# Optimization experiments

Hardware: AMD Instinct MI355X
Metric: run time of the kernel (lower is better)

Reference implementation:

```python
import jax, jax.numpy as jnp
import numpy as np

H, D = 8, 64
LN_EPS = 1e-5

def elu_p1(x):
    return jax.nn.elu(x) + 1.0

def sum_norm(x):
    return x / jnp.sum(x, axis=-1, keepdims=True)

def setup_inputs() -> dict:
    key = jax.random.key(0)
    k1, k2, k3 = jax.random.split(key, 3)
    slen, bsz, in_dim = 1024, 32, 512
    x = jax.random.normal(k1, (slen, bsz, in_dim), dtype=jnp.float32)
    ln_gamma = jnp.ones((in_dim,), dtype=jnp.float32)
    ln_beta = jnp.zeros((in_dim,), dtype=jnp.float32)
    # Linear weights stored as [in, out] (transposed vs torch) and fan-in scaled
    w_slow = jax.random.normal(k2, (in_dim, H * (3 * D + 1)), dtype=jnp.float32) / np.sqrt(in_dim)
    w_out = jax.random.normal(k3, (H * D, in_dim), dtype=jnp.float32) / np.sqrt(H * D)
    return {"x": x, "ln_gamma": ln_gamma, "ln_beta": ln_beta, "w_slow": w_slow, "w_out": w_out}

def reference(x, ln_gamma, ln_beta, w_slow, w_out):
    slen, bsz, in_dim = x.shape
    # LayerNorm
    mu = jnp.mean(x, axis=-1, keepdims=True)
    var = jnp.mean((x - mu) ** 2, axis=-1, keepdims=True)
    h = (x - mu) * jax.lax.rsqrt(var + LN_EPS) * ln_gamma + ln_beta
    # slow net projection -> q, k, v, beta per head
    qkvb = (h @ w_slow).reshape(slen, bsz, H, 3 * D + 1)
    q, k, v, beta = jnp.split(qkvb, [D, 2 * D, 3 * D], axis=-1)
    beta = jax.nn.sigmoid(beta)            # [slen, bsz, H, 1]
    q = sum_norm(elu_p1(q))                # [slen, bsz, H, D]
    k = sum_norm(elu_p1(k))
    # delta-rule fast-weight recurrence over time
    W0 = jnp.zeros((bsz, H, D, D), dtype=x.dtype)
    def step(W, inp):
        q_t, k_t, v_t, b_t = inp           # [bsz,H,D], [bsz,H,D], [bsz,H,D], [bsz,H,1]
        v_old = jnp.einsum('bhij,bhj->bhi', W, k_t)
        upd = b_t * (v_t - v_old)          # [bsz,H,D]
        W = W + upd[..., :, None] * k_t[..., None, :]
        o_t = jnp.einsum('bhij,bhj->bhi', W, q_t)
        return W, o_t
    _, outs = jax.lax.scan(step, W0, (q, k, v, beta))  # outs [slen, bsz, H, D]
    out = outs.reshape(slen, bsz, H * D) @ w_out       # [slen, bsz, in_dim]
    return x + out
```

## Files before the change

kernel.cpp:

```cpp
#include <hip/hip_runtime.h>
#include <cstdint>

using short8  = __attribute__((ext_vector_type(8))) short;
using ushort8 = __attribute__((ext_vector_type(8))) unsigned short;
using short4v = __attribute__((ext_vector_type(4))) short;
using f32x4   = __attribute__((ext_vector_type(4))) float;

#define H_    8
#define SLEN  1024
#define BSZ   32
#define INDIM 512
#define NQKV  1544
#define NPAD2 1792
#define MROWS 32768
#define PB    72

#define GLOAD16(gp, lp) __builtin_amdgcn_global_load_lds( \
    (const __attribute__((address_space(1))) void*)(gp),  \
    (__attribute__((address_space(3))) void*)(lp), 16, 0, 0)

#define VMCNT8() do { asm volatile("s_waitcnt vmcnt(8)" ::: "memory"); \
                      __builtin_amdgcn_sched_barrier(0); } while (0)
#define VMCNT0() do { asm volatile("s_waitcnt vmcnt(0)" ::: "memory"); \
                      __builtin_amdgcn_sched_barrier(0); } while (0)
#define SBAR()   do { __builtin_amdgcn_sched_barrier(0); \
                      __builtin_amdgcn_s_barrier(); \
                      __builtin_amdgcn_sched_barrier(0); } while (0)

static __device__ __forceinline__ float bf2f(unsigned short s) {
    return __uint_as_float(((unsigned int)s) << 16);
}
#if defined(__BF16_MANT_DIG__)
static __device__ __forceinline__ unsigned short f2bf(float f) {
    union { __bf16 b; unsigned short u; } cv;
    cv.b = (__bf16)f;
    return cv.u;
}
#else
static __device__ __forceinline__ unsigned short f2bf(float f) {
    unsigned int u = __float_as_uint(f);
    u += 0x7FFFu + ((u >> 16) & 1u);
    return (unsigned short)(u >> 16);
}
#endif

__global__ __launch_bounds__(256) void ln_kernel(const float* __restrict__ x,
                                                 const float* __restrict__ gamma,
                                                 const float* __restrict__ betap,
                                                 unsigned short* __restrict__ h) {
    int row = blockIdx.x * 4 + (threadIdx.x >> 6);
    int l   = threadIdx.x & 63;
    const f32x4* xr = (const f32x4*)(x + (size_t)row * INDIM);
    f32x4 a = xr[l * 2], b = xr[l * 2 + 1];
    float s = 0.f, sq = 0.f;
    #pragma unroll
    for (int j = 0; j < 4; ++j) { s += a[j]; sq += a[j] * a[j]; }
    #pragma unroll
    for (int j = 0; j < 4; ++j) { s += b[j]; sq += b[j] * b[j]; }
    #pragma unroll
    for (int off = 32; off; off >>= 1) { s += __shfl_xor(s, off); sq += __shfl_xor(sq, off); }
    float mean = s * (1.f / 512.f);
    float var  = sq * (1.f / 512.f) - mean * mean;
    float rstd = rsqrtf(var + 1e-5f);
    const f32x4* g4 = (const f32x4*)gamma;
    const f32x4* b4 = (const f32x4*)betap;
    f32x4 g0 = g4[l * 2], g1 = g4[l * 2 + 1], e0 = b4[l * 2], e1 = b4[l * 2 + 1];
    short8 o;
    #pragma unroll
    for (int j = 0; j < 4; ++j) o[j]     = (short)f2bf((a[j] - mean) * rstd * g0[j] + e0[j]);
    #pragma unroll
    for (int j = 0; j < 4; ++j) o[4 + j] = (short)f2bf((b[j] - mean) * rstd * g1[j] + e1[j]);
    ((short8*)(h + (size_t)row * INDIM))[l] = o;
}

__global__ __launch_bounds__(256) void cvt_wslow2(const float* __restrict__ w,
                                                  unsigned short* __restrict__ wT) {
    __shared__ float T[64][65];
    const int tid = threadIdx.x;
    const int k0 = blockIdx.x * 64;
    const int ng = blockIdx.y;
    if (ng < 24) {
        const int cbase = (ng & 7) * 193 + (ng >> 3) * 64;
        const int nn = tid & 63, kk = tid >> 6;
        #pragma unroll
        for (int i = 0; i < 16; ++i)
            T[kk + 4 * i][nn] = w[(size_t)(k0 + kk + 4 * i) * NQKV + cbase + nn];
        __syncthreads();
        const int kseg = (tid & 7) * 8;
        #pragma unroll
        for (int i = 0; i < 2; ++i) {
            int nn2 = i * 32 + (tid >> 3);
            ushort8 o;
            #pragma unroll
            for (int j = 0; j < 8; ++j) o[j] = f2bf(T[kseg + j][nn2]);
            *(ushort8*)&wT[(size_t)(ng * 64 + nn2) * 512 + k0 + kseg] = o;
        }
    } else {
        for (int i = 0; i < 64; ++i) {
            int gid = i * 256 + tid;
            int nn = gid >> 6, kk = gid & 63;
            int n = 1536 + nn;
            unsigned short v = 0;
            if (n < 1544) v = f2bf(w[(size_t)(k0 + kk) * NQKV + (n - 1536) * 193 + 192]);
            wT[(size_t)n * 512 + k0 + kk] = v;
        }
    }
}
__global__ __launch_bounds__(256) void cvt_wout(const float* __restrict__ w,
                                                unsigned short* __restrict__ wT) {
    __shared__ float T[64][65];
    const int tid = threadIdx.x;
    const int k0 = blockIdx.x * 64;
    const int n0 = blockIdx.y * 64;
    const int nn = tid & 63, kk = tid >> 6;
    #pragma unroll
    for (int i = 0; i < 16; ++i)
        T[kk + 4 * i][nn] = w[(size_t)(k0 + kk + 4 * i) * 512 + n0 + nn];
    __syncthreads();
    const int kseg = (tid & 7) * 8;
    #pragma unroll
    for (int i = 0; i < 2; ++i) {
        int nn2 = i * 32 + (tid >> 3);
        ushort8 o;
        #pragma unroll
        for (int j = 0; j < 8; ++j) o[j] = f2bf(T[kseg + j][nn2]);
        *(ushort8*)&wT[(size_t)(n0 + nn2) * 512 + k0 + kseg] = o;
    }
}

__global__ __launch_bounds__(512, 2) void gemm_qkv(const unsigned short* __restrict__ A,
                                                   const unsigned short* __restrict__ BT,
                                                   unsigned short* __restrict__ qn,
                                                   unsigned short* __restrict__ kn,
                                                   unsigned short* __restrict__ vn,
                                                   float* __restrict__ bet) {
    __shared__ unsigned short SMEM[65536];
    const int tid = threadIdx.x;
    const int id = blockIdx.y * 7 + blockIdx.x;
    const int newid = (id & 7) * 112 + (id >> 3);
    const int bx = newid % 7;
    const int n0 = bx * 256;
    const int m0 = (newid / 7) * 256;
    const int w = tid >> 6, l = tid & 63;
    const int wm = w >> 2, wn = w & 3;
    const int lr = l & 15, lk8 = (l >> 4) * 8;
    f32x4 acc[8][4] = {};

    auto STAGE = [&](int buf, int kt) {
        #pragma unroll
        for (int c2 = 0; c2 < 4; ++c2) {
            int idx = c2 * 512 + tid;
            int row = idx >> 3, kc2 = (idx & 7) * 8;
            int lb = (c2 * 512 + (tid & 448)) * 8;
            GLOAD16(A  + (size_t)(m0 + row) * INDIM + kt + kc2, &SMEM[buf * 16384 + lb]);
            GLOAD16(BT + (size_t)(n0 + row) * INDIM + kt + kc2, &SMEM[32768 + buf * 16384 + lb]);
        }
    };
    auto COMPUTE = [&](int buf) {
        const unsigned short* As = &SMEM[buf * 16384];
        const unsigned short* Bs = &SMEM[32768 + buf * 16384];
        short8 bf2[4][2];
        #pragma unroll
        for (int ni = 0; ni < 4; ++ni)
            #pragma unroll
            for (int kk = 0; kk < 2; ++kk)
                bf2[ni][kk] = *(const short8*)&Bs[(wn * 64 + ni * 16 + lr) * 64 + kk * 32 + lk8];
        #pragma unroll
        for (int p = 0; p < 4; ++p) {
            short8 af[2][2];
            #pragma unroll
            for (int d = 0; d < 2; ++d)
                #pragma unroll
                for (int kk = 0; kk < 2; ++kk)
                    af[d][kk] = *(const short8*)&As[(wm * 128 + (2 * p + d) * 16 + lr) * 64 + kk * 32 + lk8];
            #pragma unroll
            for (int d = 0; d < 2; ++d)
                #pragma unroll
                for (int ni = 0; ni < 4; ++ni)
                    #pragma unroll
                    for (int kk = 0; kk < 2; ++kk)
                        acc[2 * p + d][ni] =
                            __builtin_amdgcn_mfma_f32_16x16x32_bf16(af[d][kk], bf2[ni][kk], acc[2 * p + d][ni], 0, 0, 0);
        }
    };

    STAGE(0, 0);
    STAGE(1, 64);
    #pragma unroll
    for (int tp = 0; tp < 4; ++tp) {
        VMCNT8();
        SBAR();
        COMPUTE(0);
        SBAR();
        if (tp < 3) {
            STAGE(0, (2 * tp + 2) * 64);
            VMCNT8();
        } else {
            VMCNT0();
        }
        SBAR();
        COMPUTE(1);
        SBAR();
        if (tp < 3) STAGE(1, (2 * tp + 3) * 64);
    }

    const int g = l >> 4, cc = l & 15;
    const int colbase = n0 + wn * 64;
    if (bx < 6) {
        const int reg = colbase >> 9;
        #pragma unroll
        for (int mi = 0; mi < 8; ++mi) {
            #pragma unroll
            for (int j = 0; j < 4; ++j) {
                float e0 = acc[mi][0][j], e1 = acc[mi][1][j], e2 = acc[mi][2][j], e3 = acc[mi][3][j];
                if (reg < 2) {
                    e0 = e0 > 0.f ? e0 + 1.f : __expf(e0);
                    e1 = e1 > 0.f ? e1 + 1.f : __expf(e1);
                    e2 = e2 > 0.f ? e2 + 1.f : __expf(e2);
                    e3 = e3 > 0.f ? e3 + 1.f : __expf(e3);
                    float ssum = (e0 + e1) + (e2 + e3);
                    ssum += __shfl_xor(ssum, 1);
                    ssum += __shfl_xor(ssum, 2);
                    ssum += __shfl_xor(ssum, 4);
                    ssum += __shfl_xor(ssum, 8);
                    float inv = 1.f / ssum;
                    e0 *= inv; e1 *= inv; e2 *= inv; e3 *= inv;
                }
                int lrow = wm * 128 + mi * 16 + g * 4 + j;
                int key = ((lrow >> 2) & 3) << 4;
                int cb = wn * 64;
                SMEM[lrow * 256 + ((cb +  0 + cc) ^ key)] = f2bf(e0);
                SMEM[lrow * 256 + ((cb + 16 + cc) ^ key)] = f2bf(e1);
                SMEM[lrow * 256 + ((cb + 32 + cc) ^ key)] = f2bf(e2);
                SMEM[lrow * 256 + ((cb + 48 + cc) ^ key)] = f2bf(e3);
            }
        }
        SBAR();
        unsigned short* dst = (reg == 0) ? qn : (reg == 1) ? kn : vn;
        #pragma unroll
        for (int it = 0; it < 16; ++it) {
            int idx = it * 512 + tid;
            int lrow = idx >> 5, seg = idx & 31;
            int key = ((lrow >> 2) & 3) << 4;
            ushort8 v = *(const ushort8*)&SMEM[lrow * 256 + ((seg * 8) ^ key)];
            int grow = m0 + lrow;
            int s = grow >> 5, b = grow & 31;
            int gcol = n0 + seg * 8;
            int hd = (gcol >> 6) & 7, d0 = gcol & 63;
            *(ushort8*)(dst + ((size_t)(b * H_ + hd) * SLEN + s) * 64 + d0) = v;
        }
    } else {
        if (wn == 0 && cc < 8) {
            #pragma unroll
            for (int mi = 0; mi < 8; ++mi)
                #pragma unroll
                for (int j = 0; j < 4; ++j) {
                    int row = m0 + wm * 128 + mi * 16 + g * 4 + j;
                    int s = row >> 5, b = row & 31;
                    float v = acc[mi][0][j];
                    bet[(size_t)(b * H_ + cc) * SLEN + s] = 1.f / (1.f + __expf(-v));
                }
        }
    }
}

__global__ __launch_bounds__(512, 2) void gemm_out(const unsigned short* __restrict__ A,
                                                   const unsigned short* __restrict__ BT,
                                                   const float* __restrict__ X,
                                                   float* __restrict__ outf) {
    __shared__ unsigned short As[2][256 * 64];
    __shared__ unsigned short Bs[2][256 * 64];
    const int tid = threadIdx.x;
    const int id = blockIdx.y * 2 + blockIdx.x;
    const int newid = (id & 7) * 32 + (id >> 3);
    const int n0 = (newid & 1) * 256;
    const int m0 = (newid >> 1) * 256;
    const int w = tid >> 6, l = tid & 63;
    const int wm = w >> 2, wn = w & 3;
    const int lr = l & 15, lk8 = (l >> 4) * 8;
    f32x4 acc[8][4] = {};

    auto STAGE = [&](int buf, int kt) {
        #pragma unroll
        for (int c2 = 0; c2 < 4; ++c2) {
            int idx = c2 * 512 + tid;
            int row = idx >> 3, kc2 = (idx & 7) * 8;
            int lb = (c2 * 512 + (tid & 448)) * 8;
            GLOAD16(A  + (size_t)(m0 + row) * INDIM + kt + kc2, &As[buf][lb]);
            GLOAD16(BT + (size_t)(n0 + row) * INDIM + kt + kc2, &Bs[buf][lb]);
        }
    };
    auto COMPUTE = [&](int buf) {
        short8 bf2[4][2];
        #pragma unroll
        for (int ni = 0; ni < 4; ++ni)
            #pragma unroll
            for (int kk = 0; kk < 2; ++kk)
                bf2[ni][kk] = *(const short8*)&Bs[buf][(wn * 64 + ni * 16 + lr) * 64 + kk * 32 + lk8];
        #pragma unroll
        for (int p = 0; p < 4; ++p) {
            short8 af[2][2];
            #pragma unroll
            for (int d = 0; d < 2; ++d)
                #pragma unroll
                for (int kk = 0; kk < 2; ++kk)
                    af[d][kk] = *(const short8*)&As[buf][(wm * 128 + (2 * p + d) * 16 + lr) * 64 + kk * 32 + lk8];
            #pragma unroll
            for (int d = 0; d < 2; ++d)
                #pragma unroll
                for (int ni = 0; ni < 4; ++ni)
                    #pragma unroll
                    for (int kk = 0; kk < 2; ++kk)
                        acc[2 * p + d][ni] =
                            __builtin_amdgcn_mfma_f32_16x16x32_bf16(af[d][kk], bf2[ni][kk], acc[2 * p + d][ni], 0, 0, 0);
        }
    };

    STAGE(0, 0);
    STAGE(1, 64);
    #pragma unroll
    for (int tp = 0; tp < 4; ++tp) {
        VMCNT8();
        SBAR();
        COMPUTE(0);
        SBAR();
        if (tp < 3) {
            STAGE(0, (2 * tp + 2) * 64);
            VMCNT8();
        } else {
            VMCNT0();
        }
        SBAR();
        COMPUTE(1);
        SBAR();
        if (tp < 3) STAGE(1, (2 * tp + 3) * 64);
    }

    const int g = l >> 4, cc = l & 15;
    #pragma unroll
    for (int mi = 0; mi < 8; ++mi)
        #pragma unroll
        for (int ni = 0; ni < 4; ++ni)
            #pragma unroll
            for (int j = 0; j < 4; ++j) {
                int row = m0 + wm * 128 + mi * 16 + g * 4 + j;
                int col = n0 + wn * 64 + ni * 16 + cc;
                size_t o = (size_t)row * 512 + col;
                outf[o] = X[o] + acc[mi][ni][j];
            }
}

__global__ __launch_bounds__(512, 4) void fwtiles(const unsigned short* __restrict__ qn,
                                                  const unsigned short* __restrict__ kn,
                                                  const unsigned short* __restrict__ vn,
                                                  const float* __restrict__ beta,
                                                  unsigned short* __restrict__ tiles,
                                                  unsigned short* __restrict__ outs) {
    __shared__ unsigned short Ax[64 * PB], Atr[64 * PB], Pw[64 * PB], Pwtr[64 * PB];
    __shared__ unsigned short Z0[128 * PB], Z1[128 * PB];
    __shared__ float bv[64];
    const int bx = blockIdx.x;
    const int bh = bx >> 4, c = bx & 15;
    const int b = bh >> 3, h = bh & 7;
    const int c0 = c * 64;
    const int tid = threadIdx.x;
    const int w = tid >> 6, l = tid & 63;
    const int mw = w & 3, nh = w >> 2;
    const int lr = l & 15, lk = (l >> 4) << 3, rb = (l >> 4) << 2;
    const unsigned short* kc = kn + ((size_t)bh * SLEN + c0) * 64;
    const unsigned short* qc = qn + ((size_t)bh * SLEN + c0) * 64;
    const unsigned short* vc = vn + ((size_t)bh * SLEN + c0) * 64;
    const float* bb = beta + (size_t)bh * SLEN + c0;

    {
        #pragma unroll
        for (int i = 0; i < 2; ++i) {
            int idx = i * 512 + tid;
            int row = idx >> 3, seg = idx & 7;
            const unsigned short* src = (row < 64) ? (vc + (size_t)row * 64 + seg * 8)
                                                   : (kc + (size_t)(row - 64) * 64 + seg * 8);
            *(ushort8*)&Z1[row * PB + seg * 8] = *(const ushort8*)src;
        }
        if (tid < 64) bv[tid] = bb[tid];
        ushort8 z8 = {};
        for (int i = tid; i < 576; i += 512) { ((ushort8*)Ax)[i] = z8; ((ushort8*)Atr)[i] = z8; }
    }
    __syncthreads();

    auto ldb = [&](const unsigned short* M, int m, int kk) -> short8 {
        return *(const short8*)&M[(m * 16 + lr) * PB + kk * 32 + lk];
    };

    {
        const int zoff2 = (w >> 2) * 64;
        const int tbase = (w & 3) * 16;
        const float sgn = (w >= 4) ? -1.f : 1.f;
        ushort8 b0v, b1v;
        #pragma unroll
        for (int i = 0; i < 16; ++i) {
            int r = w * 16 + i;
            float val = sgn * bv[tbase + i] * bf2f(Z1[r * PB + l]);
            unsigned short uv = f2bf(val);
            if (i < 8) b0v[i] = uv; else b1v[i - 8] = uv;
        }
        *(ushort8*)&Z0[(zoff2 + l) * PB + tbase]     = b0v;
        *(ushort8*)&Z0[(zoff2 + l) * PB + tbase + 8] = b1v;
    }
    {
        const int pm[10] = {0, 1, 1, 2, 2, 2, 3, 3, 3, 3};
        const int pn[10] = {0, 0, 1, 0, 1, 2, 0, 1, 2, 3};
        for (int pi = w; pi < 10; pi += 8) {
            int m = pm[pi], n = pn[pi];
            short8 ka0 = *(const short8*)&Z1[(64 + 16 * m + lr) * PB + lk];
            short8 ka1 = *(const short8*)&Z1[(64 + 16 * m + lr) * PB + 32 + lk];
            short8 kb0 = *(const short8*)&Z1[(64 + 16 * n + lr) * PB + lk];
            short8 kb1 = *(const short8*)&Z1[(64 + 16 * n + lr) * PB + 32 + lk];
            f32x4 a = {};
            a = __builtin_amdgcn_mfma_f32_16x16x32_bf16(ka0, kb0, a, 0, 0, 0);
            a = __builtin_amdgcn_mfma_f32_16x16x32_bf16(ka1, kb1, a, 0, 0, 0);
            f32x4 btm = *(const f32x4*)&bv[16 * m + rb];
            short4v pk;
            #pragma unroll
            for (int j = 0; j < 4; ++j) {
                int tt = 16 * m + rb + j, s = 16 * n + lr;
                unsigned short v = (s < tt) ? f2bf(-btm[j] * a[j]) : (unsigned short)0;
                Ax[tt * PB + s] = v;
                pk[j] = (short)v;
            }
            *(short4v*)&Atr[(16 * n + lr) * PB + 16 * m + rb] = pk;
        }
    }
    __syncthreads();

    auto zprod = [&](const unsigned short* Xb, int p, const unsigned short* Zs, unsigned short* Zd) {
        const bool msk0 = (16 * mw + 15 >= p), msk1 = (16 * mw + 15 - 32 >= p);
        short8 xf0, xf1;
        if (msk0) xf0 = ldb(Xb, mw, 0);
        if (msk1) xf1 = ldb(Xb, mw, 1);
        #pragma unroll
        for (int ni = 0; ni < 4; ++ni) {
            int n = nh * 4 + ni;
            short4v zi = *(const short4v*)&Zs[(16 * n + lr) * PB + 16 * mw + rb];
            f32x4 a;
            #pragma unroll
            for (int j = 0; j < 4; ++j) a[j] = bf2f((unsigned short)zi[j]);
            if (msk0) a = __builtin_amdgcn_mfma_f32_16x16x32_bf16(xf0, ldb(Zs, n, 0), a, 0, 0, 0);
            if (msk1) a = __builtin_amdgcn_mfma_f32_16x16x32_bf16(xf1, ldb(Zs, n, 1), a, 0, 0, 0);
            short4v zo;
            #pragma unroll
            for (int j = 0; j < 4; ++j) zo[j] = (short)f2bf(a[j]);
            *(short4v*)&Zd[(16 * n + lr) * PB + 16 * mw + rb] = zo;
        }
    };
    auto powp = [&](const unsigned short* Ps, const unsigned short* Pstr, int p,
                    unsigned short* Pd, unsigned short* Pdtr, bool wrTr) {
        const bool x0 = (16 * mw + 15 >= p), x1 = (16 * mw + 15 - 32 >= p);
        short8 xf0, xf1;
        if (x0) xf0 = ldb(Ps, mw, 0);
        if (x1) xf1 = ldb(Ps, mw, 1);
        #pragma unroll
        for (int ni = 0; ni < 2; ++ni) {
            int n = nh * 2 + ni;
            const bool y0 = (31 - 16 * n >= p), y1 = (63 - 16 * n >= p);
            f32x4 a = {};
            if (x0 && y0) a = __builtin_amdgcn_mfma_f32_16x16x32_bf16(xf0, ldb(Pstr, n, 0), a, 0, 0, 0);
            if (x1 && y1) a = __builtin_amdgcn_mfma_f32_16x16x32_bf16(xf1, ldb(Pstr, n, 1), a, 0, 0, 0);
            short4v pk;
            #pragma unroll
            for (int j = 0; j < 4; ++j) {
                unsigned short v = f2bf(a[j]);
                Pd[(16 * mw + rb + j) * PB + 16 * n + lr] = v;
                pk[j] = (short)v;
            }
            if (wrTr) *(short4v*)&Pdtr[(16 * n + lr) * PB + 16 * mw + rb] = pk;
        }
    };

    zprod(Ax, 1, Z0, Z1);  powp(Ax, Atr, 1, Pw, Pwtr, true);   __syncthreads();
    zprod(Pw, 2, Z1, Z0);  powp(Pw, Pwtr, 2, Ax, Atr, true);   __syncthreads();
    zprod(Ax, 4, Z0, Z1);  powp(Ax, Atr, 4, Pw, Pwtr, true);   __syncthreads();
    zprod(Pw, 8, Z1, Z0);  powp(Pw, Pwtr, 8, Ax, Atr, true);   __syncthreads();
    zprod(Ax, 16, Z0, Z1); powp(Ax, Atr, 16, Pw, Pwtr, false); __syncthreads();
    zprod(Pw, 32, Z1, Z0);
    __syncthreads();

    {
        #pragma unroll
        for (int i = 0; i < 2; ++i) {
            int idx = i * 512 + tid;
            int row = idx >> 3, seg = idx & 7;
            const unsigned short* src = (row < 64) ? (qc + (size_t)row * 64 + seg * 8)
                                                   : (kc + (size_t)(row - 64) * 64 + seg * 8);
            *(ushort8*)&Z1[row * PB + seg * 8] = *(const ushort8*)src;
        }
    }
    __syncthreads();

    {
        short8 qa0 = *(const short8*)&Z1[(16 * mw + lr) * PB + lk];
        short8 qa1 = *(const short8*)&Z1[(16 * mw + lr) * PB + 32 + lk];
        #pragma unroll
        for (int ni = 0; ni < 2; ++ni) {
            int n = nh * 2 + ni;
            short8 kb0 = *(const short8*)&Z1[(64 + 16 * n + lr) * PB + lk];
            short8 kb1 = *(const short8*)&Z1[(64 + 16 * n + lr) * PB + 32 + lk];
            f32x4 a = {};
            a = __builtin_amdgcn_mfma_f32_16x16x32_bf16(qa0, kb0, a, 0, 0, 0);
            a = __builtin_amdgcn_mfma_f32_16x16x32_bf16(qa1, kb1, a, 0, 0, 0);
            #pragma unroll
            for (int j = 0; j < 4; ++j) {
                int tt = 16 * mw + rb + j, s = 16 * n + lr;
                Ax[tt * PB + s] = (s <= tt) ? f2bf(a[j]) : (unsigned short)0;
            }
        }
        ushort8 kv;
        #pragma unroll
        for (int j = 0; j < 8; ++j)
            kv[j] = Z1[(64 + w * 8 + j) * PB + l];
        *(ushort8*)&Pwtr[l * PB + w * 8] = kv;
    }
    __syncthreads();

    {
        unsigned short* tb = tiles + ((size_t)bh * 16 + c) * 12288;
        short8 pA0 = ldb(Ax, mw, 0), pA1 = ldb(Ax, mw, 1);
        short8 zA0 = ldb(Z0, mw, 0), zA1 = ldb(Z0, mw, 1);
        short8 kt0 = ldb(Pwtr, mw, 0), kt1 = ldb(Pwtr, mw, 1);
        #pragma unroll
        for (int ni = 0; ni < 2; ++ni) {
            int n = nh * 2 + ni;
            f32x4 aN = {};
            aN = __builtin_amdgcn_mfma_f32_16x16x32_bf16(zA0, ldb(Pwtr, n, 0), aN, 0, 0, 0);
            aN = __builtin_amdgcn_mfma_f32_16x16x32_bf16(zA1, ldb(Pwtr, n, 1), aN, 0, 0, 0);
            f32x4 aM = {};
            aM = __builtin_amdgcn_mfma_f32_16x16x32_bf16(kt0, ldb(Z0, 4 + n, 0), aM, 0, 0, 0);
            aM = __builtin_amdgcn_mfma_f32_16x16x32_bf16(kt1, ldb(Z0, 4 + n, 1), aM, 0, 0, 0);
            f32x4 aG;
            #pragma unroll
            for (int j = 0; j < 4; ++j) aG[j] = bf2f(Z1[(16 * mw + rb + j) * PB + 16 * n + lr]);
            aG = __builtin_amdgcn_mfma_f32_16x16x32_bf16(pA0, ldb(Z0, 4 + n, 0), aG, 0, 0, 0);
            aG = __builtin_amdgcn_mfma_f32_16x16x32_bf16(pA1, ldb(Z0, 4 + n, 1), aG, 0, 0, 0);
            f32x4 aP = {};
            aP = __builtin_amdgcn_mfma_f32_16x16x32_bf16(pA0, ldb(Z0, n, 0), aP, 0, 0, 0);
            aP = __builtin_amdgcn_mfma_f32_16x16x32_bf16(pA1, ldb(Z0, n, 1), aP, 0, 0, 0);
            #pragma unroll
            for (int j = 0; j < 4; ++j) {
                int r = 16 * mw + rb + j, cl = 16 * n + lr;
                tb[r * 64 + cl]        = f2bf(aM[j]);
                tb[4096 + r * 64 + cl] = f2bf(aG[j]);
                tb[8192 + r * 64 + cl] = f2bf(aN[j]);
                outs[((size_t)(c0 + r) * BSZ + b) * 512 + h * 64 + cl] = f2bf(aP[j]);
            }
        }
    }
}

__global__ __launch_bounds__(256) void fwscan_w(const unsigned short* __restrict__ tiles,
                                                unsigned short* __restrict__ wchk) {
    __shared__ float Wf[64 * 68];
    const int bh = blockIdx.x;
    const int tid = threadIdx.x;
    const int w = tid >> 6, l = tid & 63;
    const int lr = l & 15, lk = (l >> 4) << 3, rb = (l >> 4) << 2;
    const int cr = l >> 3, cc8 = (l & 7) * 8;
    #pragma unroll
    for (int j = 0; j < 16; ++j) Wf[(16 * w + j) * 68 + l] = 0.f;

    const unsigned short* tb0 = tiles + (size_t)bh * 16 * 12288;
    unsigned short* wc0 = wchk + (size_t)bh * 16 * 4096;

    auto loadc = [&](short8 (&MT)[4][2], unsigned short (&NV)[4][4], int c) {
        const unsigned short* tb = tb0 + (size_t)c * 12288;
        #pragma unroll
        for (int n = 0; n < 4; ++n) {
            MT[n][0] = *(const short8*)(tb + (size_t)(16 * n + lr) * 64 + lk);
            MT[n][1] = *(const short8*)(tb + (size_t)(16 * n + lr) * 64 + 32 + lk);
            #pragma unroll
            for (int j = 0; j < 4; ++j)
                NV[n][j] = tb[8192 + (size_t)(16 * w + rb + j) * 64 + 16 * n + lr];
        }
    };
    auto stepc = [&](short8 (&MT)[4][2], unsigned short (&NV)[4][4], int c) {
        #pragma unroll
        for (int half = 0; half < 2; ++half) {
            int row = 16 * w + half * 8 + cr;
            const float* p = &Wf[row * 68 + cc8];
            f32x4 x0 = *(const f32x4*)p, x1 = *(const f32x4*)(p + 4);
            ushort8 o;
            #pragma unroll
            for (int j = 0; j < 4; ++j) { o[j] = f2bf(x0[j]); o[4 + j] = f2bf(x1[j]); }
            *(ushort8*)(wc0 + (size_t)c * 4096 + row * 64 + cc8) = o;
        }
        short8 wf0, wf1;
        {
            const float* p0 = &Wf[(16 * w + lr) * 68 + lk];
            f32x4 a0 = *(const f32x4*)p0, b0 = *(const f32x4*)(p0 + 4);
            f32x4 a1 = *(const f32x4*)(p0 + 32), b1 = *(const f32x4*)(p0 + 36);
            #pragma unroll
            for (int j = 0; j < 4; ++j) {
                wf0[j] = (short)f2bf(a0[j]); wf0[4 + j] = (short)f2bf(b0[j]);
                wf1[j] = (short)f2bf(a1[j]); wf1[4 + j] = (short)f2bf(b1[j]);
            }
        }
        #pragma unroll
        for (int n = 0; n < 4; ++n) {
            f32x4 a;
            #pragma unroll
            for (int j = 0; j < 4; ++j)
                a[j] = Wf[(16 * w + rb + j) * 68 + 16 * n + lr] + bf2f(NV[n][j]);
            a = __builtin_amdgcn_mfma_f32_16x16x32_bf16(wf0, MT[n][0], a, 0, 0, 0);
            a = __builtin_amdgcn_mfma_f32_16x16x32_bf16(wf1, MT[n][1], a, 0, 0, 0);
            #pragma unroll
            for (int j = 0; j < 4; ++j) Wf[(16 * w + rb + j) * 68 + 16 * n + lr] = a[j];
        }
    };

    short8 mtA[4][2], mtB[4][2];
    unsigned short nvA[4][4], nvB[4][4];
    loadc(mtA, nvA, 0);
    #pragma unroll 1
    for (int cc = 0; cc < 8; ++cc) {
        int c = 2 * cc;
        if (c + 1 < 16) loadc(mtB, nvB, c + 1);
        stepc(mtA, nvA, c);
        if (c + 2 < 16) loadc(mtA, nvA, c + 2);
        stepc(mtB, nvB, c + 1);
    }
}

__global__ __launch_bounds__(256) void fw_o(const unsigned short* __restrict__ tiles,
                                            const unsigned short* __restrict__ wchk,
                                            unsigned short* __restrict__ outs) {
    __shared__ unsigned short Ot[64 * 72];
    const int c = blockIdx.x + 1;
    const int bh = blockIdx.y;
    const int b = bh >> 3, h = bh & 7;
    const int c0 = c * 64;
    const int tid = threadIdx.x;
    const int w = tid >> 6, l = tid & 63;
    const int lr = l & 15, lk = (l >> 4) << 3, rb = (l >> 4) << 2;
    const unsigned short* G  = tiles + ((size_t)bh * 16 + c) * 12288 + 4096;
    const unsigned short* W0 = wchk + ((size_t)bh * 16 + c) * 4096;

    #pragma unroll
    for (int i = 0; i < 2; ++i) {
        int idx = i * 256 + tid;
        int t = idx >> 3, d0 = (idx & 7) * 8;
        *(ushort8*)&Ot[t * 72 + d0] =
            *(const ushort8*)(outs + ((size_t)(c0 + t) * BSZ + b) * 512 + h * 64 + d0);
    }
    __syncthreads();

    short8 g0 = *(const short8*)(G + (size_t)(16 * w + lr) * 64 + lk);
    short8 g1 = *(const short8*)(G + (size_t)(16 * w + lr) * 64 + 32 + lk);
    #pragma unroll
    for (int n = 0; n < 4; ++n) {
        short8 wf0 = *(const short8*)(W0 + (size_t)(16 * n + lr) * 64 + lk);
        short8 wf1 = *(const short8*)(W0 + (size_t)(16 * n + lr) * 64 + 32 + lk);
        f32x4 a;
        #pragma unroll
        for (int j = 0; j < 4; ++j) a[j] = bf2f(Ot[(16 * w + rb + j) * 72 + 16 * n + lr]);
        a = __builtin_amdgcn_mfma_f32_16x16x32_bf16(g0, wf0, a, 0, 0, 0);
        a = __builtin_amdgcn_mfma_f32_16x16x32_bf16(g1, wf1, a, 0, 0, 0);
        #pragma unroll
        for (int j = 0; j < 4; ++j) Ot[(16 * w + rb + j) * 72 + 16 * n + lr] = f2bf(a[j]);
    }
    __syncthreads();

    #pragma unroll
    for (int i = 0; i < 2; ++i) {
        int idx = i * 256 + tid;
        int t = idx >> 3, d0 = (idx & 7) * 8;
        *(ushort8*)(outs + ((size_t)(c0 + t) * BSZ + b) * 512 + h * 64 + d0) =
            *(const ushort8*)&Ot[t * 72 + d0];
    }
}

extern "C" void kernel_launch(void* const* d_in, const int* in_sizes, int n_in,
                              void* d_out, int out_size, void* d_ws, size_t ws_size,
                              hipStream_t stream) {
    const float* x      = (const float*)d_in[0];
    const float* g      = (const float*)d_in[1];
    const float* be     = (const float*)d_in[2];
    const float* w_slow = (const float*)d_in[3];
    const float* w_out  = (const float*)d_in[4];
    float* out = (float*)d_out;
    char* ws = (char*)d_ws;

    unsigned short* h    = (unsigned short*)(ws);
    unsigned short* outs = (unsigned short*)(ws);
    unsigned short* qn   = (unsigned short*)(ws + 33554432);
    unsigned short* wchk = (unsigned short*)(ws + 33554432);
    unsigned short* kn   = (unsigned short*)(ws + 67108864);
    unsigned short* vn   = (unsigned short*)(ws + 100663296);
    float*          bet  = (float*)         (ws + 134217728);
    unsigned short* wsT  = (unsigned short*)(ws + 135266304);
    unsigned short* woT  = (unsigned short*)(ws + 137101312);
    unsigned short* tiles= (unsigned short*)(ws + 137625600);

    if (ws_size < 238288896) return;

    ln_kernel<<<8192, 256, 0, stream>>>(x, g, be, h);
    cvt_wslow2<<<dim3(8, 25), 256, 0, stream>>>(w_slow, wsT);
    cvt_wout<<<dim3(8, 8), 256, 0, stream>>>(w_out, woT);
    gemm_qkv<<<dim3(7, MROWS / 256), 512, 0, stream>>>(h, wsT, qn, kn, vn, bet);
    fwtiles<<<BSZ * H_ * 16, 512, 0, stream>>>(qn, kn, vn, bet, tiles, outs);
    fwscan_w<<<BSZ * H_, 256, 0, stream>>>(tiles, wchk);
    fw_o<<<dim3(15, BSZ * H_), 256, 0, stream>>>(tiles, wchk, outs);
    gemm_out<<<dim3(2, MROWS / 256), 512, 0, stream>>>(outs, woT, x, out);
}
```

Baseline: 339.8 us.

## Halve GEMM K-tile to 32 to cut LDS and raise occupancy

Result: slower. 780.0 us (+129.6%).

```diff
diff --git a/kernel.cpp b/kernel.cpp
--- a/kernel.cpp
+++ b/kernel.cpp
@@ -1,4 +1,5 @@
 #include <hip/hip_runtime.h>
+#include <hip/hip_bf16.h>
 #include <cstdint>
 
 using short8  = __attribute__((ext_vector_type(8))) short;
@@ -19,7 +20,7 @@
     (const __attribute__((address_space(1))) void*)(gp),  \
     (__attribute__((address_space(3))) void*)(lp), 16, 0, 0)
 
-#define VMCNT8() do { asm volatile("s_waitcnt vmcnt(8)" ::: "memory"); \
+#define VMCNT4() do { asm volatile("s_waitcnt vmcnt(4)" ::: "memory"); \
                       __builtin_amdgcn_sched_barrier(0); } while (0)
 #define VMCNT0() do { asm volatile("s_waitcnt vmcnt(0)" ::: "memory"); \
                       __builtin_amdgcn_sched_barrier(0); } while (0)
@@ -30,19 +31,11 @@
 static __device__ __forceinline__ float bf2f(unsigned short s) {
     return __uint_as_float(((unsigned int)s) << 16);
 }
-#if defined(__BF16_MANT_DIG__)
 static __device__ __forceinline__ unsigned short f2bf(float f) {
-    union { __bf16 b; unsigned short u; } cv;
-    cv.b = (__bf16)f;
+    union { __hip_bfloat16 b; unsigned short u; } cv;
+    cv.b = __float2bfloat16(f);
     return cv.u;
 }
-#else
-static __device__ __forceinline__ unsigned short f2bf(float f) {
-    unsigned int u = __float_as_uint(f);
-    u += 0x7FFFu + ((u >> 16) & 1u);
-    return (unsigned short)(u >> 16);
-}
-#endif
 
 __global__ __launch_bounds__(256) void ln_kernel(const float* __restrict__ x,
                                                  const float* __restrict__ gamma,
@@ -128,13 +121,13 @@
     }
 }
 
-__global__ __launch_bounds__(512, 2) void gemm_qkv(const unsigned short* __restrict__ A,
+__global__ __launch_bounds__(512, 4) void gemm_qkv(const unsigned short* __restrict__ A,
                                                    const unsigned short* __restrict__ BT,
                                                    unsigned short* __restrict__ qn,
                                                    unsigned short* __restrict__ kn,
                                                    unsigned short* __restrict__ vn,
                                                    float* __restrict__ bet) {
-    __shared__ unsigned short SMEM[65536];
+    __shared__ unsigned short SMEM[32768];
     const int tid = threadIdx.x;
     const int id = blockIdx.y * 7 + blockIdx.x;
     const int newid = (id & 7) * 112 + (id >> 3);
@@ -148,106 +141,97 @@
 
     auto STAGE = [&](int buf, int kt) {
         #pragma unroll
-        for (int c2 = 0; c2 < 4; ++c2) {
+        for (int c2 = 0; c2 < 2; ++c2) {
             int idx = c2 * 512 + tid;
-            int row = idx >> 3, kc2 = (idx & 7) * 8;
+            int row = idx >> 2, kc2 = (idx & 3) * 8;
             int lb = (c2 * 512 + (tid & 448)) * 8;
-            GLOAD16(A  + (size_t)(m0 + row) * INDIM + kt + kc2, &SMEM[buf * 16384 + lb]);
-            GLOAD16(BT + (size_t)(n0 + row) * INDIM + kt + kc2, &SMEM[32768 + buf * 16384 + lb]);
+            GLOAD16(A  + (size_t)(m0 + row) * INDIM + kt + kc2, &SMEM[buf * 8192 + lb]);
+            GLOAD16(BT + (size_t)(n0 + row) * INDIM + kt + kc2, &SMEM[16384 + buf * 8192 + lb]);
         }
     };
     auto COMPUTE = [&](int buf) {
-        const unsigned short* As = &SMEM[buf * 16384];
-        const unsigned short* Bs = &SMEM[32768 + buf * 16384];
-        short8 bf2[4][2];
+        const unsigned short* As = &SMEM[buf * 8192];
+        const unsigned short* Bs = &SMEM[16384 + buf * 8192];
+        short8 bf2[4];
         #pragma unroll
         for (int ni = 0; ni < 4; ++ni)
-            #pragma unroll
-            for (int kk = 0; kk < 2; ++kk)
-                bf2[ni][kk] = *(const short8*)&Bs[(wn * 64 + ni * 16 + lr) * 64 + kk * 32 + lk8];
+            bf2[ni] = *(const short8*)&Bs[(wn * 64 + ni * 16 + lr) * 32 + lk8];
         #pragma unroll
         for (int p = 0; p < 4; ++p) {
-            short8 af[2][2];
+            short8 af[2];
             #pragma unroll
             for (int d = 0; d < 2; ++d)
-                #pragma unroll
-                for (int kk = 0; kk < 2; ++kk)
-                    af[d][kk] = *(const short8*)&As[(wm * 128 + (2 * p + d) * 16 + lr) * 64 + kk * 32 + lk8];
+                af[d] = *(const short8*)&As[(wm * 128 + (2 * p + d) * 16 + lr) * 32 + lk8];
             #pragma unroll
             for (int d = 0; d < 2; ++d)
                 #pragma unroll
                 for (int ni = 0; ni < 4; ++ni)
-                    #pragma unroll
-                    for (int kk = 0; kk < 2; ++kk)
-                        acc[2 * p + d][ni] =
-                            __builtin_amdgcn_mfma_f32_16x16x32_bf16(af[d][kk], bf2[ni][kk], acc[2 * p + d][ni], 0, 0, 0);
+                    acc[2 * p + d][ni] =
+                        __builtin_amdgcn_mfma_f32_16x16x32_bf16(af[d], bf2[ni], acc[2 * p + d][ni], 0, 0, 0);
         }
     };
 
     STAGE(0, 0);
-    STAGE(1, 64);
-    #pragma unroll
-    for (int tp = 0; tp < 4; ++tp) {
-        VMCNT8();
+    STAGE(1, 32);
+    #pragma unroll
+    for (int t = 0; t < 16; ++t) {
+        if (t == 15) { VMCNT0(); } else { VMCNT4(); }
         SBAR();
-        COMPUTE(0);
+        COMPUTE(t & 1);
         SBAR();
-        if (tp < 3) {
-            STAGE(0, (2 * tp + 2) * 64);
-            VMCNT8();
-        } else {
-            VMCNT0();
-        }
-        SBAR();
-        COMPUTE(1);
-        SBAR();
-        if (tp < 3) STAGE(1, (2 * tp + 3) * 64);
+        if (t + 2 < 16) STAGE(t & 1, (t + 2) * 32);
     }
 
     const int g = l >> 4, cc = l & 15;
     const int colbase = n0 + wn * 64;
     if (bx < 6) {
         const int reg = colbase >> 9;
-        #pragma unroll
-        for (int mi = 0; mi < 8; ++mi) {
-            #pragma unroll
-            for (int j = 0; j < 4; ++j) {
-                float e0 = acc[mi][0][j], e1 = acc[mi][1][j], e2 = acc[mi][2][j], e3 = acc[mi][3][j];
-                if (reg < 2) {
-                    e0 = e0 > 0.f ? e0 + 1.f : __expf(e0);
-                    e1 = e1 > 0.f ? e1 + 1.f : __expf(e1);
-                    e2 = e2 > 0.f ? e2 + 1.f : __expf(e2);
-                    e3 = e3 > 0.f ? e3 + 1.f : __expf(e3);
-                    float ssum = (e0 + e1) + (e2 + e3);
-                    ssum += __shfl_xor(ssum, 1);
-                    ssum += __shfl_xor(ssum, 2);
-                    ssum += __shfl_xor(ssum, 4);
-                    ssum += __shfl_xor(ssum, 8);
-                    float inv = 1.f / ssum;
-                    e0 *= inv; e1 *= inv; e2 *= inv; e3 *= inv;
+        unsigned short* dst = (reg == 0) ? qn : (reg == 1) ? kn : vn;
+        #pragma unroll
+        for (int hp = 0; hp < 2; ++hp) {
+            SBAR();
+            if (wm == hp) {
+                #pragma unroll
+                for (int mi = 0; mi < 8; ++mi) {
+                    #pragma unroll
+                    for (int j = 0; j < 4; ++j) {
+                        float e0 = acc[mi][0][j], e1 = acc[mi][1][j], e2 = acc[mi][2][j], e3 = acc[mi][3][j];
+                        if (reg < 2) {
+                            e0 = e0 > 0.f ? e0 + 1.f : __expf(e0);
+                            e1 = e1 > 0.f ? e1 + 1.f : __expf(e1);
+                            e2 = e2 > 0.f ? e2 + 1.f : __expf(e2);
+                            e3 = e3 > 0.f ? e3 + 1.f : __expf(e3);
+                            float ssum = (e0 + e1) + (e2 + e3);
+                            ssum += __shfl_xor(ssum, 1);
+                            ssum += __shfl_xor(ssum, 2);
+                            ssum += __shfl_xor(ssum, 4);
+                            ssum += __shfl_xor(ssum, 8);
+                            float inv = 1.f / ssum;
+                            e0 *= inv; e1 *= inv; e2 *= inv; e3 *= inv;
+                        }
+                        int lrow = mi * 16 + g * 4 + j;
+                        int key = ((lrow >> 2) & 3) << 4;
+                        int cb = wn * 64;
+                        SMEM[lrow * 256 + ((cb +  0 + cc) ^ key)] = f2bf(e0);
+                        SMEM[lrow * 256 + ((cb + 16 + cc) ^ key)] = f2bf(e1);
+                        SMEM[lrow * 256 + ((cb + 32 + cc) ^ key)] = f2bf(e2);
+                        SMEM[lrow * 256 + ((cb + 48 + cc) ^ key)] = f2bf(e3);
+                    }
                 }
-                int lrow = wm * 128 + mi * 16 + g * 4 + j;
+            }
+            SBAR();
+            #pragma unroll
+            for (int it = 0; it < 8; ++it) {
+                int idx = it * 512 + tid;
+                int lrow = idx >> 5, seg = idx & 31;
                 int key = ((lrow >> 2) & 3) << 4;
-                int cb = wn * 64;
-                SMEM[lrow * 256 + ((cb +  0 + cc) ^ key)] = f2bf(e0);
-                SMEM[lrow * 256 + ((cb + 16 + cc) ^ key)] = f2bf(e1);
-                SMEM[lrow * 256 + ((cb + 32 + cc) ^ key)] = f2bf(e2);
-                SMEM[lrow * 256 + ((cb + 48 + cc) ^ key)] = f2bf(e3);
-            }
-        }
-        SBAR();
-        unsigned short* dst = (reg == 0) ? qn : (reg == 1) ? kn : vn;
-        #pragma unroll
-        for (int it = 0; it < 16; ++it) {
-            int idx = it * 512 + tid;
-            int lrow = idx >> 5, seg = idx & 31;
-            int key = ((lrow >> 2) & 3) << 4;
-            ushort8 v = *(const ushort8*)&SMEM[lrow * 256 + ((seg * 8) ^ key)];
-            int grow = m0 + lrow;
-            int s = grow >> 5, b = grow & 31;
-            int gcol = n0 + seg * 8;
-            int hd = (gcol >> 6) & 7, d0 = gcol & 63;
-            *(ushort8*)(dst + ((size_t)(b * H_ + hd) * SLEN + s) * 64 + d0) = v;
+                ushort8 v = *(const ushort8*)&SMEM[lrow * 256 + ((seg * 8) ^ key)];
+                int grow = m0 + hp * 128 + lrow;
+                int s = grow >> 5, b = grow & 31;
+                int gcol = n0 + seg * 8;
+                int hd = (gcol >> 6) & 7, d0 = gcol & 63;
+                *(ushort8*)(dst + ((size_t)(b * H_ + hd) * SLEN + s) * 64 + d0) = v;
+            }
         }
     } else {
         if (wn == 0 && cc < 8) {
@@ -264,12 +248,12 @@
     }
 }
 
-__global__ __launch_bounds__(512, 2) void gemm_out(const unsigned short* __restrict__ A,
+__global__ __launch_bounds__(512, 4) void gemm_out(const unsigned short* __restrict__ A,
                                                    const unsigned short* __restrict__ BT,
                                                    const float* __restrict__ X,
                                                    float* __restrict__ outf) {
-    __shared__ unsigned short As[2][256 * 64];
-    __shared__ unsigned short Bs[2][256 * 64];
+    __shared__ unsigned short As2[2][8192];
+    __shared__ unsigned short Bs2[2][8192];
     const int tid = threadIdx.x;
     const int id = blockIdx.y * 2 + blockIdx.x;
     const int newid = (id & 7) * 32 + (id >> 3);
@@ -282,58 +266,43 @@
 
     auto STAGE = [&](int buf, int kt) {
         #pragma unroll
-        for (int c2 = 0; c2 < 4; ++c2) {
+        for (int c2 = 0; c2 < 2; ++c2) {
             int idx = c2 * 512 + tid;
-            int row = idx >> 3, kc2 = (idx & 7) * 8;
+            int row = idx >> 2, kc2 = (idx & 3) * 8;
             int lb = (c2 * 512 + (tid & 448)) * 8;
-            GLOAD16(A  + (size_t)(m0 + row) * INDIM + kt + kc2, &As[buf][lb]);
-            GLOAD16(BT + (size_t)(n0 + row) * INDIM + kt + kc2, &Bs[buf][lb]);
+            GLOAD16(A  + (size_t)(m0 + row) * INDIM + kt + kc2, &As2[buf][lb]);
+            GLOAD16(BT + (size_t)(n0 + row) * INDIM + kt + kc2, &Bs2[buf][lb]);
         }
     };
     auto COMPUTE = [&](int buf) {
-        short8 bf2[4][2];
+        short8 bf2[4];
         #pragma unroll
         for (int ni = 0; ni < 4; ++ni)
-            #pragma unroll
-            for (int kk = 0; kk < 2; ++kk)
-                bf2[ni][kk] = *(const short8*)&Bs[buf][(wn * 64 + ni * 16 + lr) * 64 + kk * 32 + lk8];
+            bf2[ni] = *(const short8*)&Bs2[buf][(wn * 64 + ni * 16 + lr) * 32 + lk8];
         #pragma unroll
         for (int p = 0; p < 4; ++p) {
-            short8 af[2][2];
+            short8 af[2];
             #pragma unroll
             for (int d = 0; d < 2; ++d)
-                #pragma unroll
-                for (int kk = 0; kk < 2; ++kk)
-                    af[d][kk] = *(const short8*)&As[buf][(wm * 128 + (2 * p + d) * 16 + lr) * 64 + kk * 32 + lk8];
+                af[d] = *(const short8*)&As2[buf][(wm * 128 + (2 * p + d) * 16 + lr) * 32 + lk8];
             #pragma unroll
             for (int d = 0; d < 2; ++d)
                 #pragma unroll
                 for (int ni = 0; ni < 4; ++ni)
-                    #pragma unroll
-                    for (int kk = 0; kk < 2; ++kk)
-                        acc[2 * p + d][ni] =
-                            __builtin_amdgcn_mfma_f32_16x16x32_bf16(af[d][kk], bf2[ni][kk], acc[2 * p + d][ni], 0, 0, 0);
+                    acc[2 * p + d][ni] =
+                        __builtin_amdgcn_mfma_f32_16x16x32_bf16(af[d], bf2[ni], acc[2 * p + d][ni], 0, 0, 0);
         }
     };
 
     STAGE(0, 0);
-    STAGE(1, 64);
-    #pragma unroll
-    for (int tp = 0; tp < 4; ++tp) {
-        VMCNT8();
+    STAGE(1, 32);
+    #pragma unroll
+    for (int t = 0; t < 16; ++t) {
+        if (t == 15) { VMCNT0(); } else { VMCNT4(); }
         SBAR();
-        COMPUTE(0);
+        COMPUTE(t & 1);
         SBAR();
-        if (tp < 3) {
-            STAGE(0, (2 * tp + 2) * 64);
-            VMCNT8();
-        } else {
-            VMCNT0();
-        }
-        SBAR();
-        COMPUTE(1);
-        SBAR();
-        if (tp < 3) STAGE(1, (2 * tp + 3) * 64);
+        if (t + 2 < 16) STAGE(t & 1, (t + 2) * 32);
     }
 
     const int g = l >> 4, cc = l & 15;
```
